# Performance work log

Measured on AMD Instinct MI355X. Metric: run time of the kernel, lower is better.

The kernel has to match this reference:

```python
import jax, jax.numpy as jnp
import numpy as np

NSAMPLE = 16
LEAKY_RATE = 0.1


def _knn(xyz, k):
    # xyz: [B,N,3] -> idx of k nearest neighbors (incl. self): [B,N,k]
    sq = jnp.sum(xyz * xyz, axis=-1)  # [B,N]
    dist = sq[:, :, None] + sq[:, None, :] - 2.0 * jnp.einsum('bnd,bmd->bnm', xyz, xyz)
    _, idx = jax.lax.top_k(-dist, k)
    return idx


def _gather(feat, idx):
    # feat [B,N,C], idx [B,N,K] -> [B,N,K,C]
    return jax.vmap(lambda f, i: f[i])(feat, idx)


def setup_inputs() -> dict:
    key = jax.random.key(0)
    ks = jax.random.split(key, 10)
    B, N, D = 8, 4096, 61
    in_ch, out_ch, wnet = 64, 64, 16
    inp = {
        'xyz': jax.random.normal(ks[0], (B, 3, N), dtype=jnp.float32),
        'points': jax.random.normal(ks[1], (B, D, N), dtype=jnp.float32),
        # WeightNet: 1x1 convs 3->8->8->16 (hidden_unit=[8,8]), no BN
        'w0': jax.random.normal(ks[2], (8, 3), dtype=jnp.float32) * 0.3,
        'b0': jnp.zeros((8,), dtype=jnp.float32),
        'w1': jax.random.normal(ks[3], (8, 8), dtype=jnp.float32) * 0.3,
        'b1': jnp.zeros((8,), dtype=jnp.float32),
        'w2': jax.random.normal(ks[4], (wnet, 8), dtype=jnp.float32) * 0.3,
        'b2': jnp.zeros((wnet,), dtype=jnp.float32),
        # final Linear: weightnet*in_channel -> out_channel (torch [out,in] layout)
        'lin_w': jax.random.normal(ks[5], (out_ch, wnet * in_ch), dtype=jnp.float32) * 0.03,
        'lin_b': jnp.zeros((out_ch,), dtype=jnp.float32),
    }
    return inp


def reference(xyz, points, w0, b0, w1, b1, w2, b2, lin_w, lin_b):
    B, _, N = xyz.shape
    xyz_t = jnp.transpose(xyz, (0, 2, 1))     # [B,N,3]
    pts_t = jnp.transpose(points, (0, 2, 1))  # [B,N,D]
    idx = _knn(xyz_t, NSAMPLE)                # [B,N,K]
    g_xyz = _gather(xyz_t, idx) - xyz_t[:, :, None, :]   # [B,N,K,3] relative coords
    g_pts = _gather(pts_t, idx)                           # [B,N,K,D]
    new_points = jnp.concatenate([g_xyz, g_pts], axis=-1)  # [B,N,K,C], C=D+3
    # WeightNet: per-neighbor 1x1-conv MLP with ReLU on relative coords
    h = jax.nn.relu(jnp.einsum('bnkc,oc->bnko', g_xyz, w0) + b0)
    h = jax.nn.relu(jnp.einsum('bnkc,oc->bnko', h, w1) + b1)
    w = jax.nn.relu(jnp.einsum('bnkc,oc->bnko', h, w2) + b2)  # [B,N,K,W]
    # aggregate: [B,N,C,K] @ [B,N,K,W] -> [B,N,C,W] -> flatten C*W (W fastest)
    agg = jnp.einsum('bnkc,bnkw->bncw', new_points, w).reshape(B, N, -1)
    out = agg @ lin_w.T + lin_b          # [B,N,out_ch]
    out = jnp.transpose(out, (0, 2, 1))  # [B,out_ch,N]
    return jnp.where(out > 0, out, LEAKY_RATE * out)  # LeakyReLU(0.1)
```

## Files before the change

kernel.cpp:

```cpp
#include <hip/hip_runtime.h>
#include <hip/hip_bf16.h>

#define NBATCH 8
#define NP     4096
#define ND     61
#define NK     16
#define BN     (NBATCH*NP)

#define OFF_XYZT  0
#define OFF_IDX   (OFF_XYZT + BN*16)
#define OFF_PTST  (OFF_IDX + BN*64)
#define OFF_BFRAG (OFF_PTST + BN*256)

typedef __attribute__((ext_vector_type(8))) short bf16x8;
typedef __attribute__((ext_vector_type(4))) float f32x4;

static __device__ __forceinline__ unsigned short f2bf(float x) {
    unsigned int u = __float_as_uint(x);
    return (unsigned short)((u + 0x7fffu + ((u >> 16) & 1u)) >> 16);
}

__global__ __launch_bounds__(256) void k_prep(const float* __restrict__ xyz,
                                              const float* __restrict__ pts,
                                              const float* __restrict__ lw,
                                              float4* __restrict__ xyzt,
                                              float* __restrict__ ptst,
                                              uint4* __restrict__ bfrag) {
#pragma clang fp contract(off)
    __shared__ float tile[64][65];
    int blk = blockIdx.x;
    int tid = threadIdx.x;
    if (blk < 128) {
        int t = blk * 256 + tid;
        int b = t >> 12, n = t & (NP - 1);
        const float* base = xyz + (size_t)b * 3 * NP + n;
        float x = base[0], y = base[NP], z = base[2 * NP];
        float sq = ((x * x) + (y * y)) + (z * z);
        xyzt[t] = make_float4(x, y, z, sq);
    } else if (blk < 640) {
        int bb = blk - 128;
        int b = bb >> 6; int n0 = (bb & 63) << 6;
        int rg = tid >> 6; int cl = tid & 63;
#pragma unroll
        for (int d0 = 0; d0 < 64; d0 += 4) {
            int d = d0 + rg;
            if (d < ND) tile[d][cl] = pts[((size_t)b * ND + d) * NP + n0 + cl];
        }
        __syncthreads();
#pragma unroll
        for (int r = 0; r < 16; ++r) {
            int n1 = r * 4 + rg;
            float v = (cl < ND) ? tile[cl][n1] : 0.0f;
            ptst[((size_t)b * NP + n0 + n1) * 64 + cl] = v;
        }
    } else {
        int e = (blk - 640) * 256 + tid;
        int lane = e & 63, nt = (e >> 6) & 3, ks = e >> 8;
        int k0 = ks * 32 + (lane >> 4) * 8;
        int n = nt * 16 + (lane & 15);
        const float* src = lw + (size_t)n * 1024 + k0;
        unsigned int pk[4];
#pragma unroll
        for (int i = 0; i < 4; ++i)
            pk[i] = ((unsigned int)f2bf(src[2 * i + 1]) << 16) | f2bf(src[2 * i]);
        bfrag[e] = make_uint4(pk[0], pk[1], pk[2], pk[3]);
    }
}

#define INSERT16(dv, jv)                                            \
    do {                                                            \
        bd[15] = (dv); bi[15] = (jv);                               \
        _Pragma("unroll")                                           \
        for (int s_ = 15; s_ > 0; --s_) {                           \
            bool sw_ = bd[s_] < bd[s_ - 1];                         \
            float td_ = bd[s_]; int ti_ = bi[s_];                   \
            bd[s_]     = sw_ ? bd[s_ - 1] : td_;                    \
            bi[s_]     = sw_ ? bi[s_ - 1] : ti_;                    \
            bd[s_ - 1] = sw_ ? td_ : bd[s_ - 1];                    \
            bi[s_ - 1] = sw_ ? ti_ : bi[s_ - 1];                    \
        }                                                           \
    } while (0)

#define DRAIN16(basev)                                                        \
    do {                                                                      \
        for (int r_ = 0; r_ < 16; ++r_) {                                     \
            if (!__any(r_ < cnt)) break;                                      \
            if (r_ < cnt) {                                                   \
                int loc_ = ring[r_ * 64 + lane];                              \
                float4 cd_ = tile[loc_];                                      \
                float dot_ = __fadd_rn(__fadd_rn(__fmul_rn(cd_.x, me.x),      \
                                                 __fmul_rn(cd_.y, me.y)),     \
                                       __fmul_rn(cd_.z, me.z));               \
                float dist_ = __fsub_rn(__fadd_rn(me.w, cd_.w),               \
                                        __fmul_rn(2.0f, dot_));               \
                if (dist_ < bd[15]) {                                         \
                    int gj_ = (basev) + loc_;                                 \
                    INSERT16(dist_, gj_);                                     \
                }                                                             \
            }                                                                 \
        }                                                                     \
        cnt = 0;                                                              \
        T = fminf(T, (bd[15] - me.w) + 1.0e-3f);                              \
    } while (0)

#define TSYNC()                                                               \
    do {                                                                      \
        Tsh[w * 64 + lane] = bd[15];                                          \
        float tm_ = Tsh[lane];                                                \
        _Pragma("unroll")                                                     \
        for (int v_ = 1; v_ < 8; ++v_) tm_ = fminf(tm_, Tsh[v_ * 64 + lane]); \
        T = fminf(T, (tm_ - me.w) + 1.0e-3f);                                 \
    } while (0)

__global__ __launch_bounds__(512) void k_knn(const float4* __restrict__ xyzt,
                                             int* __restrict__ out) {
    __shared__ char smem[51200];
    int tid = threadIdx.x;
    int w = tid >> 6, lane = tid & 63;
    int blk = blockIdx.x;
    int b = blk >> 6;
    int qbase = (blk & 63) << 6;
    const float4* xb = xyzt + (size_t)b * NP;

    float4* tile = (float4*)(smem + w * 4096);
    unsigned short* ring = (unsigned short*)(smem + 32768 + w * 2048);
    float* Tsh = (float*)(smem + 49152);

    float4 me = xb[qbase + lane];
    float bd[16]; int bi[16];
#pragma unroll
    for (int i = 0; i < 16; ++i) { bd[i] = 3.0e38f; bi[i] = 0; }
    int cnt = 0;
    float T = 3.0e38f;
    Tsh[w * 64 + lane] = 3.0e38f;
    __syncthreads();

    int cbase = w * 512;
    for (int half = 0; half < 2; ++half) {
        int base = cbase + half * 256;
#pragma unroll
        for (int r = 0; r < 4; ++r)
            tile[lane + r * 64] = xb[base + lane + r * 64];
        for (int seg = 0; seg < 4; ++seg) {
            for (int g = 0; g < 8; ++g) {
                int j0 = seg * 64 + g * 8;
#pragma unroll
                for (int u = 0; u < 8; ++u) {
                    int jj = j0 + u;
                    float4 cd = tile[jj];
                    float dotf = fmaf(cd.z, me.z, fmaf(cd.y, me.y, cd.x * me.x));
                    float df = fmaf(-2.0f, dotf, cd.w);
                    if (df < T) { ring[cnt * 64 + lane] = (unsigned short)jj; ++cnt; }
                }
                if (__any(cnt >= 8)) { DRAIN16(base); }
                if (half == 0 && seg == 0 && (g == 1 || g == 3)) { TSYNC(); }
            }
            TSYNC();
        }
        DRAIN16(base);
    }

    __syncthreads();
    float2* part = (float2*)smem;
    if (w < 4) {
#pragma unroll
        for (int e = 0; e < 16; ++e)
            part[(w * 16 + e) * 64 + lane] = make_float2(bd[e], __int_as_float(bi[e]));
    }
    __syncthreads();
    if (w == 0) {
        for (int s = 1; s < 4; ++s) {
#pragma unroll
            for (int e = 0; e < 16; ++e) {
                float2 v = part[(s * 16 + e) * 64 + lane];
                if (v.x >= bd[15]) break;
                float d_ = v.x; int j_ = __float_as_int(v.y);
                INSERT16(d_, j_);
            }
        }
    }
    __syncthreads();
    if (w >= 4) {
#pragma unroll
        for (int e = 0; e < 16; ++e)
            part[((w - 4) * 16 + e) * 64 + lane] = make_float2(bd[e], __int_as_float(bi[e]));
    }
    __syncthreads();
    if (w == 0) {
        for (int s = 0; s < 4; ++s) {
#pragma unroll
            for (int e = 0; e < 16; ++e) {
                float2 v = part[(s * 16 + e) * 64 + lane];
                if (v.x >= bd[15]) break;
                float d_ = v.x; int j_ = __float_as_int(v.y);
                INSERT16(d_, j_);
            }
        }
        int4* op = (int4*)(out + ((size_t)b * NP + qbase + lane) * 16);
        op[0] = make_int4(bi[0], bi[1], bi[2], bi[3]);
        op[1] = make_int4(bi[4], bi[5], bi[6], bi[7]);
        op[2] = make_int4(bi[8], bi[9], bi[10], bi[11]);
        op[3] = make_int4(bi[12], bi[13], bi[14], bi[15]);
    }
}

__global__ __launch_bounds__(256) void k_wagg(
    const float4* __restrict__ xyzt, const int* __restrict__ knn,
    const float* __restrict__ ptst, const uint4* __restrict__ bfrag,
    const float* __restrict__ w0, const float* __restrict__ b0,
    const float* __restrict__ w1, const float* __restrict__ b1,
    const float* __restrict__ w2, const float* __restrict__ b2,
    const float* __restrict__ linb, float* __restrict__ out) {
    __shared__ float wkl[256 * 16];
    __shared__ float4 rel4[256];
    __shared__ uint4 aggL4[16 * 128];
    char* aggL = (char*)aggL4;

    int tid = threadIdx.x;
    int wid = tid >> 6, lane = tid & 63;
    int q0 = blockIdx.x * 16;
    int b = q0 >> 12;
    int n0 = q0 & (NP - 1);
    size_t bN = (size_t)b * NP;

    {
        int pw = lane >> 4, k = lane & 15;
        int p = wid * 4 + pw;
        int r = p * 16 + k;
        int q = q0 + p;
        int j = knn[(size_t)q * 16 + k];
        float4 pj = xyzt[bN + j];
        float4 pq = xyzt[q];
        float rx = pj.x - pq.x, ry = pj.y - pq.y, rz = pj.z - pq.z;
        float h0[8], h1[8], wv[16];
#pragma unroll
        for (int o = 0; o < 8; ++o) {
            float a = w0[o * 3 + 0] * rx + w0[o * 3 + 1] * ry + w0[o * 3 + 2] * rz + b0[o];
            h0[o] = a > 0.0f ? a : 0.0f;
        }
#pragma unroll
        for (int o = 0; o < 8; ++o) {
            float a = b1[o];
#pragma unroll
            for (int c2 = 0; c2 < 8; ++c2) a += w1[o * 8 + c2] * h0[c2];
            h1[o] = a > 0.0f ? a : 0.0f;
        }
#pragma unroll
        for (int o = 0; o < 16; ++o) {
            float a = b2[o];
#pragma unroll
            for (int c2 = 0; c2 < 8; ++c2) a += w2[o * 8 + c2] * h1[c2];
            wv[o] = a > 0.0f ? a : 0.0f;
        }
        int f = (r >> 1) & 3;
#pragma unroll
        for (int s = 0; s < 4; ++s)
            *(float4*)&wkl[r * 16 + ((s ^ f) << 2)] =
                make_float4(wv[s * 4], wv[s * 4 + 1], wv[s * 4 + 2], wv[s * 4 + 3]);
        rel4[r] = make_float4(rx, ry, rz, __int_as_float(j));
    }
    __syncthreads();

    for (int u = 0; u < 4; ++u) {
        int p = wid * 4 + u;
        float acc[16];
#pragma unroll
        for (int w = 0; w < 16; ++w) acc[w] = 0.0f;
#pragma unroll
        for (int kh = 0; kh < 2; ++kh) {
            float vv[8];
#pragma unroll
            for (int kk = 0; kk < 8; ++kk) {
                int r = p * 16 + kh * 8 + kk;
                float4 rj = rel4[r];
                int j = __float_as_int(rj.w);
                vv[kk] = (lane >= 3) ? ptst[(bN + j) * 64 + (lane - 3)]
                                     : ((lane == 0) ? rj.x : ((lane == 1) ? rj.y : rj.z));
            }
#pragma unroll
            for (int kk = 0; kk < 8; ++kk) {
                int r = p * 16 + kh * 8 + kk;
                int f = (r >> 1) & 3;
                float v = vv[kk];
#pragma unroll
                for (int s = 0; s < 4; ++s) {
                    float4 wv4 = *(const float4*)&wkl[r * 16 + ((s ^ f) << 2)];
                    acc[s * 4 + 0] = fmaf(v, wv4.x, acc[s * 4 + 0]);
                    acc[s * 4 + 1] = fmaf(v, wv4.y, acc[s * 4 + 1]);
                    acc[s * 4 + 2] = fmaf(v, wv4.z, acc[s * 4 + 2]);
                    acc[s * 4 + 3] = fmaf(v, wv4.w, acc[s * 4 + 3]);
                }
            }
        }
        unsigned int pk[8];
#pragma unroll
        for (int i = 0; i < 8; ++i)
            pk[i] = ((unsigned int)f2bf(acc[2 * i + 1]) << 16) | f2bf(acc[2 * i]);
        int cx = lane ^ (p & 7);
        *(uint4*)&aggL[p * 2048 + cx * 16]        = make_uint4(pk[0], pk[1], pk[2], pk[3]);
        *(uint4*)&aggL[p * 2048 + 1024 + cx * 16] = make_uint4(pk[4], pk[5], pk[6], pk[7]);
    }
    __syncthreads();

    f32x4 cacc = {0.0f, 0.0f, 0.0f, 0.0f};
    {
        int p_ = lane & 15, oct = lane >> 4;
        int h = oct & 1, chalf = oct >> 1;
        int pbase = p_ * 2048 + h * 1024;
        int px = p_ & 7;
#pragma unroll 4
        for (int ks = 0; ks < 32; ++ks) {
            int c = ks * 2 + chalf;
            bf16x8 av = *(const bf16x8*)&aggL[pbase + ((c ^ px) << 4)];
            bf16x8 bv = *(const bf16x8*)&bfrag[(ks * 4 + wid) * 64 + lane];
            cacc = __builtin_amdgcn_mfma_f32_16x16x32_bf16(av, bv, cacc, 0, 0, 0);
        }
    }
    __syncthreads();
    float* cout = wkl;
    {
        int o = wid * 16 + (lane & 15);
        int rbase = (lane >> 4) * 4;
#pragma unroll
        for (int reg = 0; reg < 4; ++reg)
            cout[o * 17 + rbase + reg] = cacc[reg];
    }
    __syncthreads();
    {
        int oo = tid >> 2, pq = tid & 3;
        float bias = linb[oo];
        float res[4];
#pragma unroll
        for (int e = 0; e < 4; ++e) {
            float s = cout[oo * 17 + pq * 4 + e] + bias;
            res[e] = s > 0.0f ? s : 0.1f * s;
        }
        *(float4*)&out[((size_t)(b * 64 + oo)) * NP + n0 + pq * 4] =
            make_float4(res[0], res[1], res[2], res[3]);
    }
}

extern "C" void kernel_launch(void* const* d_in, const int* in_sizes, int n_in,
                              void* d_out, int out_size, void* d_ws, size_t ws_size,
                              hipStream_t stream) {
    const float* xyz  = (const float*)d_in[0];
    const float* pts  = (const float*)d_in[1];
    const float* w0   = (const float*)d_in[2];
    const float* b0   = (const float*)d_in[3];
    const float* w1   = (const float*)d_in[4];
    const float* b1   = (const float*)d_in[5];
    const float* w2   = (const float*)d_in[6];
    const float* b2   = (const float*)d_in[7];
    const float* lw   = (const float*)d_in[8];
    const float* linb = (const float*)d_in[9];
    float* out = (float*)d_out;

    char* ws = (char*)d_ws;
    float4* xyzt  = (float4*)(ws + OFF_XYZT);
    int*    idx   = (int*)(ws + OFF_IDX);
    float*  ptst  = (float*)(ws + OFF_PTST);
    uint4*  bfrag = (uint4*)(ws + OFF_BFRAG);

    k_prep<<<672, 256, 0, stream>>>(xyz, pts, lw, xyzt, ptst, bfrag);
    k_knn<<<512, 512, 0, stream>>>(xyzt, idx);
    k_wagg<<<BN / 16, 256, 0, stream>>>(xyzt, idx, ptst, bfrag,
                                        w0, b0, w1, b1, w2, b2, linb, out);
    (void)in_sizes; (void)n_in; (void)out_size; (void)ws_size;
}
```

Measured before the change: 222.8 us.

## Fuse kNN search with weightnet aggregation and linear into one kernel

Merges the kNN kernel and the weight/aggregate/MFMA kernel into a single 512-thread block that keeps the 64 queries' neighbor indices in shared memory as 16-bit values and processes them in four 16-query chunks. This removes the global index write/read and one kernel launch. In exchange, the aggregation phase runs on a grid of only 512 blocks, with half the waves idle during weightnet and MFMA. The candidate insertion in the scan loop is also changed to an unconditional ring write with a predicated counter increment, to avoid divergent branches.

```diff
diff --git a/kernel.cpp b/kernel.cpp
--- a/kernel.cpp
+++ b/kernel.cpp
@@ -112,231 +112,230 @@
         T = fminf(T, (tm_ - me.w) + 1.0e-3f);                                 \
     } while (0)
 
-__global__ __launch_bounds__(512) void k_knn(const float4* __restrict__ xyzt,
-                                             int* __restrict__ out) {
-    __shared__ char smem[51200];
-    int tid = threadIdx.x;
-    int w = tid >> 6, lane = tid & 63;
-    int blk = blockIdx.x;
-    int b = blk >> 6;
-    int qbase = (blk & 63) << 6;
-    const float4* xb = xyzt + (size_t)b * NP;
-
-    float4* tile = (float4*)(smem + w * 4096);
-    unsigned short* ring = (unsigned short*)(smem + 32768 + w * 2048);
-    float* Tsh = (float*)(smem + 49152);
-
-    float4 me = xb[qbase + lane];
-    float bd[16]; int bi[16];
-#pragma unroll
-    for (int i = 0; i < 16; ++i) { bd[i] = 3.0e38f; bi[i] = 0; }
-    int cnt = 0;
-    float T = 3.0e38f;
-    Tsh[w * 64 + lane] = 3.0e38f;
-    __syncthreads();
-
-    int cbase = w * 512;
-    for (int half = 0; half < 2; ++half) {
-        int base = cbase + half * 256;
-#pragma unroll
-        for (int r = 0; r < 4; ++r)
-            tile[lane + r * 64] = xb[base + lane + r * 64];
-        for (int seg = 0; seg < 4; ++seg) {
-            for (int g = 0; g < 8; ++g) {
-                int j0 = seg * 64 + g * 8;
-#pragma unroll
-                for (int u = 0; u < 8; ++u) {
-                    int jj = j0 + u;
-                    float4 cd = tile[jj];
-                    float dotf = fmaf(cd.z, me.z, fmaf(cd.y, me.y, cd.x * me.x));
-                    float df = fmaf(-2.0f, dotf, cd.w);
-                    if (df < T) { ring[cnt * 64 + lane] = (unsigned short)jj; ++cnt; }
-                }
-                if (__any(cnt >= 8)) { DRAIN16(base); }
-                if (half == 0 && seg == 0 && (g == 1 || g == 3)) { TSYNC(); }
-            }
-            TSYNC();
-        }
-        DRAIN16(base);
-    }
-
-    __syncthreads();
-    float2* part = (float2*)smem;
-    if (w < 4) {
-#pragma unroll
-        for (int e = 0; e < 16; ++e)
-            part[(w * 16 + e) * 64 + lane] = make_float2(bd[e], __int_as_float(bi[e]));
-    }
-    __syncthreads();
-    if (w == 0) {
-        for (int s = 1; s < 4; ++s) {
-#pragma unroll
-            for (int e = 0; e < 16; ++e) {
-                float2 v = part[(s * 16 + e) * 64 + lane];
-                if (v.x >= bd[15]) break;
-                float d_ = v.x; int j_ = __float_as_int(v.y);
-                INSERT16(d_, j_);
-            }
-        }
-    }
-    __syncthreads();
-    if (w >= 4) {
-#pragma unroll
-        for (int e = 0; e < 16; ++e)
-            part[((w - 4) * 16 + e) * 64 + lane] = make_float2(bd[e], __int_as_float(bi[e]));
-    }
-    __syncthreads();
-    if (w == 0) {
-        for (int s = 0; s < 4; ++s) {
-#pragma unroll
-            for (int e = 0; e < 16; ++e) {
-                float2 v = part[(s * 16 + e) * 64 + lane];
-                if (v.x >= bd[15]) break;
-                float d_ = v.x; int j_ = __float_as_int(v.y);
-                INSERT16(d_, j_);
-            }
-        }
-        int4* op = (int4*)(out + ((size_t)b * NP + qbase + lane) * 16);
-        op[0] = make_int4(bi[0], bi[1], bi[2], bi[3]);
-        op[1] = make_int4(bi[4], bi[5], bi[6], bi[7]);
-        op[2] = make_int4(bi[8], bi[9], bi[10], bi[11]);
-        op[3] = make_int4(bi[12], bi[13], bi[14], bi[15]);
-    }
-}
-
-__global__ __launch_bounds__(256) void k_wagg(
-    const float4* __restrict__ xyzt, const int* __restrict__ knn,
-    const float* __restrict__ ptst, const uint4* __restrict__ bfrag,
+__global__ __launch_bounds__(512, 4) void k_fused(
+    const float4* __restrict__ xyzt, const float* __restrict__ ptst,
+    const uint4* __restrict__ bfrag,
     const float* __restrict__ w0, const float* __restrict__ b0,
     const float* __restrict__ w1, const float* __restrict__ b1,
     const float* __restrict__ w2, const float* __restrict__ b2,
     const float* __restrict__ linb, float* __restrict__ out) {
-    __shared__ float wkl[256 * 16];
-    __shared__ float4 rel4[256];
-    __shared__ uint4 aggL4[16 * 128];
-    char* aggL = (char*)aggL4;
-
+    __shared__ char smem[54272];
     int tid = threadIdx.x;
-    int wid = tid >> 6, lane = tid & 63;
-    int q0 = blockIdx.x * 16;
-    int b = q0 >> 12;
-    int n0 = q0 & (NP - 1);
+    int blk = blockIdx.x;
+    int w = tid >> 6, lane = tid & 63;
+    int b = blk >> 6;
+    int qbase = (blk & 63) << 6;
+    const float4* xb = xyzt + (size_t)b * NP;
     size_t bN = (size_t)b * NP;
+    unsigned short* idxL = (unsigned short*)(smem + 52224);
 
     {
-        int pw = lane >> 4, k = lane & 15;
-        int p = wid * 4 + pw;
-        int r = p * 16 + k;
-        int q = q0 + p;
-        int j = knn[(size_t)q * 16 + k];
-        float4 pj = xyzt[bN + j];
-        float4 pq = xyzt[q];
-        float rx = pj.x - pq.x, ry = pj.y - pq.y, rz = pj.z - pq.z;
-        float h0[8], h1[8], wv[16];
-#pragma unroll
-        for (int o = 0; o < 8; ++o) {
-            float a = w0[o * 3 + 0] * rx + w0[o * 3 + 1] * ry + w0[o * 3 + 2] * rz + b0[o];
-            h0[o] = a > 0.0f ? a : 0.0f;
-        }
-#pragma unroll
-        for (int o = 0; o < 8; ++o) {
-            float a = b1[o];
-#pragma unroll
-            for (int c2 = 0; c2 < 8; ++c2) a += w1[o * 8 + c2] * h0[c2];
-            h1[o] = a > 0.0f ? a : 0.0f;
-        }
-#pragma unroll
-        for (int o = 0; o < 16; ++o) {
-            float a = b2[o];
-#pragma unroll
-            for (int c2 = 0; c2 < 8; ++c2) a += w2[o * 8 + c2] * h1[c2];
-            wv[o] = a > 0.0f ? a : 0.0f;
-        }
-        int f = (r >> 1) & 3;
-#pragma unroll
-        for (int s = 0; s < 4; ++s)
-            *(float4*)&wkl[r * 16 + ((s ^ f) << 2)] =
-                make_float4(wv[s * 4], wv[s * 4 + 1], wv[s * 4 + 2], wv[s * 4 + 3]);
-        rel4[r] = make_float4(rx, ry, rz, __int_as_float(j));
+        float4* tile = (float4*)(smem + w * 4096);
+        unsigned short* ring = (unsigned short*)(smem + 32768 + w * 2048);
+        float* Tsh = (float*)(smem + 49152);
+
+        float4 me = xb[qbase + lane];
+        float bd[16]; int bi[16];
+#pragma unroll
+        for (int i = 0; i < 16; ++i) { bd[i] = 3.0e38f; bi[i] = 0; }
+        int cnt = 0;
+        float T = 3.0e38f;
+        Tsh[w * 64 + lane] = 3.0e38f;
+        __syncthreads();
+
+        int cbase = w * 512;
+        for (int half = 0; half < 2; ++half) {
+            int base = cbase + half * 256;
+#pragma unroll
+            for (int r = 0; r < 4; ++r)
+                tile[lane + r * 64] = xb[base + lane + r * 64];
+            for (int seg = 0; seg < 4; ++seg) {
+                for (int g = 0; g < 8; ++g) {
+                    int j0 = seg * 64 + g * 8;
+#pragma unroll
+                    for (int u = 0; u < 8; ++u) {
+                        int jj = j0 + u;
+                        float4 cd = tile[jj];
+                        float dotf = fmaf(cd.z, me.z, fmaf(cd.y, me.y, cd.x * me.x));
+                        float df = fmaf(-2.0f, dotf, cd.w);
+                        ring[cnt * 64 + lane] = (unsigned short)jj;
+                        cnt += (df < T) ? 1 : 0;
+                    }
+                    if (__any(cnt >= 8)) { DRAIN16(base); }
+                    if (half == 0 && seg == 0 && (g == 1 || g == 3)) { TSYNC(); }
+                }
+                TSYNC();
+            }
+            DRAIN16(base);
+        }
+
+        __syncthreads();
+        float2* part = (float2*)smem;
+        if (w < 4) {
+#pragma unroll
+            for (int e = 0; e < 16; ++e)
+                part[(w * 16 + e) * 64 + lane] = make_float2(bd[e], __int_as_float(bi[e]));
+        }
+        __syncthreads();
+        if (w == 0) {
+            for (int s = 1; s < 4; ++s) {
+#pragma unroll
+                for (int e = 0; e < 16; ++e) {
+                    float2 v = part[(s * 16 + e) * 64 + lane];
+                    if (v.x >= bd[15]) break;
+                    float d_ = v.x; int j_ = __float_as_int(v.y);
+                    INSERT16(d_, j_);
+                }
+            }
+        }
+        __syncthreads();
+        if (w >= 4) {
+#pragma unroll
+            for (int e = 0; e < 16; ++e)
+                part[((w - 4) * 16 + e) * 64 + lane] = make_float2(bd[e], __int_as_float(bi[e]));
+        }
+        __syncthreads();
+        if (w == 0) {
+            for (int s = 0; s < 4; ++s) {
+#pragma unroll
+                for (int e = 0; e < 16; ++e) {
+                    float2 v = part[(s * 16 + e) * 64 + lane];
+                    if (v.x >= bd[15]) break;
+                    float d_ = v.x; int j_ = __float_as_int(v.y);
+                    INSERT16(d_, j_);
+                }
+            }
+#pragma unroll
+            for (int e = 0; e < 16; ++e)
+                idxL[lane * 16 + e] = (unsigned short)bi[e];
+        }
     }
     __syncthreads();
 
-    for (int u = 0; u < 4; ++u) {
-        int p = wid * 4 + u;
-        float acc[16];
-#pragma unroll
-        for (int w = 0; w < 16; ++w) acc[w] = 0.0f;
-#pragma unroll
-        for (int kh = 0; kh < 2; ++kh) {
-            float vv[8];
-#pragma unroll
-            for (int kk = 0; kk < 8; ++kk) {
-                int r = p * 16 + kh * 8 + kk;
-                float4 rj = rel4[r];
-                int j = __float_as_int(rj.w);
-                vv[kk] = (lane >= 3) ? ptst[(bN + j) * 64 + (lane - 3)]
-                                     : ((lane == 0) ? rj.x : ((lane == 1) ? rj.y : rj.z));
-            }
-#pragma unroll
-            for (int kk = 0; kk < 8; ++kk) {
-                int r = p * 16 + kh * 8 + kk;
-                int f = (r >> 1) & 3;
-                float v = vv[kk];
-#pragma unroll
-                for (int s = 0; s < 4; ++s) {
-                    float4 wv4 = *(const float4*)&wkl[r * 16 + ((s ^ f) << 2)];
-                    acc[s * 4 + 0] = fmaf(v, wv4.x, acc[s * 4 + 0]);
-                    acc[s * 4 + 1] = fmaf(v, wv4.y, acc[s * 4 + 1]);
-                    acc[s * 4 + 2] = fmaf(v, wv4.z, acc[s * 4 + 2]);
-                    acc[s * 4 + 3] = fmaf(v, wv4.w, acc[s * 4 + 3]);
-                }
-            }
-        }
-        unsigned int pk[8];
-#pragma unroll
-        for (int i = 0; i < 8; ++i)
-            pk[i] = ((unsigned int)f2bf(acc[2 * i + 1]) << 16) | f2bf(acc[2 * i]);
-        int cx = lane ^ (p & 7);
-        *(uint4*)&aggL[p * 2048 + cx * 16]        = make_uint4(pk[0], pk[1], pk[2], pk[3]);
-        *(uint4*)&aggL[p * 2048 + 1024 + cx * 16] = make_uint4(pk[4], pk[5], pk[6], pk[7]);
-    }
-    __syncthreads();
-
-    f32x4 cacc = {0.0f, 0.0f, 0.0f, 0.0f};
-    {
-        int p_ = lane & 15, oct = lane >> 4;
-        int h = oct & 1, chalf = oct >> 1;
-        int pbase = p_ * 2048 + h * 1024;
-        int px = p_ & 7;
+    float* wkl  = (float*)smem;
+    float* relx = (float*)(smem + 16384);
+    float* rely = (float*)(smem + 17408);
+    float* relz = (float*)(smem + 18432);
+    char*  aggL = smem + 19456;
+
+    for (int c = 0; c < 4; ++c) {
+        int n0 = qbase + c * 16;
+
+        if (tid < 256) {
+            int pw = lane >> 4, k = lane & 15;
+            int p = (tid >> 6) * 4 + pw;
+            int r = p * 16 + k;
+            int j = idxL[(c * 16 + p) * 16 + k];
+            float4 pj = xb[j];
+            float4 pq = xb[n0 + p];
+            float rx = pj.x - pq.x, ry = pj.y - pq.y, rz = pj.z - pq.z;
+            float h0[8], h1[8], wv[16];
+#pragma unroll
+            for (int o = 0; o < 8; ++o) {
+                float a = w0[o * 3 + 0] * rx + w0[o * 3 + 1] * ry + w0[o * 3 + 2] * rz + b0[o];
+                h0[o] = a > 0.0f ? a : 0.0f;
+            }
+#pragma unroll
+            for (int o = 0; o < 8; ++o) {
+                float a = b1[o];
+#pragma unroll
+                for (int c2 = 0; c2 < 8; ++c2) a += w1[o * 8 + c2] * h0[c2];
+                h1[o] = a > 0.0f ? a : 0.0f;
+            }
+#pragma unroll
+            for (int o = 0; o < 16; ++o) {
+                float a = b2[o];
+#pragma unroll
+                for (int c2 = 0; c2 < 8; ++c2) a += w2[o * 8 + c2] * h1[c2];
+                wv[o] = a > 0.0f ? a : 0.0f;
+            }
+            int f = (r >> 1) & 3;
+#pragma unroll
+            for (int s = 0; s < 4; ++s)
+                *(float4*)&wkl[r * 16 + ((s ^ f) << 2)] =
+                    make_float4(wv[s * 4], wv[s * 4 + 1], wv[s * 4 + 2], wv[s * 4 + 3]);
+            relx[r] = rx; rely[r] = ry; relz[r] = rz;
+        }
+        __syncthreads();
+
+        for (int u = 0; u < 2; ++u) {
+            int p = w * 2 + u;
+            float acc[16];
+#pragma unroll
+            for (int q = 0; q < 16; ++q) acc[q] = 0.0f;
+#pragma unroll
+            for (int kh = 0; kh < 2; ++kh) {
+                float vv[8];
+#pragma unroll
+                for (int kk = 0; kk < 8; ++kk) {
+                    int r = p * 16 + kh * 8 + kk;
+                    int j = idxL[(c * 16 + p) * 16 + kh * 8 + kk];
+                    vv[kk] = (lane >= 3) ? ptst[(bN + j) * 64 + (lane - 3)]
+                                         : ((lane == 0) ? relx[r]
+                                                        : ((lane == 1) ? rely[r] : relz[r]));
+                }
+#pragma unroll
+                for (int kk = 0; kk < 8; ++kk) {
+                    int r = p * 16 + kh * 8 + kk;
+                    int f = (r >> 1) & 3;
+                    float v = vv[kk];
+#pragma unroll
+                    for (int s = 0; s < 4; ++s) {
+                        float4 wv4 = *(const float4*)&wkl[r * 16 + ((s ^ f) << 2)];
+                        acc[s * 4 + 0] = fmaf(v, wv4.x, acc[s * 4 + 0]);
+                        acc[s * 4 + 1] = fmaf(v, wv4.y, acc[s * 4 + 1]);
+                        acc[s * 4 + 2] = fmaf(v, wv4.z, acc[s * 4 + 2]);
+                        acc[s * 4 + 3] = fmaf(v, wv4.w, acc[s * 4 + 3]);
+                    }
+                }
+            }
+            unsigned int pk[8];
+#pragma unroll
+            for (int i = 0; i < 8; ++i)
+                pk[i] = ((unsigned int)f2bf(acc[2 * i + 1]) << 16) | f2bf(acc[2 * i]);
+            int cx = lane ^ (p & 7);
+            *(uint4*)&aggL[p * 2048 + cx * 16]        = make_uint4(pk[0], pk[1], pk[2], pk[3]);
+            *(uint4*)&aggL[p * 2048 + 1024 + cx * 16] = make_uint4(pk[4], pk[5], pk[6], pk[7]);
+        }
+        __syncthreads();
+
+        f32x4 cacc = {0.0f, 0.0f, 0.0f, 0.0f};
+        if (w < 4) {
+            int p_ = lane & 15, oct = lane >> 4;
+            int h = oct & 1, chalf = oct >> 1;
+            int pbase = p_ * 2048 + h * 1024;
+            int px = p_ & 7;
 #pragma unroll 4
-        for (int ks = 0; ks < 32; ++ks) {
-            int c = ks * 2 + chalf;
-            bf16x8 av = *(const bf16x8*)&aggL[pbase + ((c ^ px) << 4)];
-            bf16x8 bv = *(const bf16x8*)&bfrag[(ks * 4 + wid) * 64 + lane];
-            cacc = __builtin_amdgcn_mfma_f32_16x16x32_bf16(av, bv, cacc, 0, 0, 0);
-        }
-    }
-    __syncthreads();
-    float* cout = wkl;
-    {
-        int o = wid * 16 + (lane & 15);
-        int rbase = (lane >> 4) * 4;
-#pragma unroll
-        for (int reg = 0; reg < 4; ++reg)
-            cout[o * 17 + rbase + reg] = cacc[reg];
-    }
-    __syncthreads();
-    {
-        int oo = tid >> 2, pq = tid & 3;
-        float bias = linb[oo];
-        float res[4];
-#pragma unroll
-        for (int e = 0; e < 4; ++e) {
-            float s = cout[oo * 17 + pq * 4 + e] + bias;
-            res[e] = s > 0.0f ? s : 0.1f * s;
-        }
-        *(float4*)&out[((size_t)(b * 64 + oo)) * NP + n0 + pq * 4] =
-            make_float4(res[0], res[1], res[2], res[3]);
+            for (int ks = 0; ks < 32; ++ks) {
+                int cc = ks * 2 + chalf;
+                bf16x8 av = *(const bf16x8*)&aggL[pbase + ((cc ^ px) << 4)];
+                bf16x8 bv = *(const bf16x8*)&bfrag[(ks * 4 + w) * 64 + lane];
+                cacc = __builtin_amdgcn_mfma_f32_16x16x32_bf16(av, bv, cacc, 0, 0, 0);
+            }
+        }
+        __syncthreads();
+        float* cout = wkl;
+        if (w < 4) {
+            int o = w * 16 + (lane & 15);
+            int rbase = (lane >> 4) * 4;
+#pragma unroll
+            for (int reg = 0; reg < 4; ++reg)
+                cout[o * 17 + rbase + reg] = cacc[reg];
+        }
+        __syncthreads();
+        if (tid < 256) {
+            int oo = tid >> 2, pq = tid & 3;
+            float bias = linb[oo];
+            float res[4];
+#pragma unroll
+            for (int e = 0; e < 4; ++e) {
+                float s = cout[oo * 17 + pq * 4 + e] + bias;
+                res[e] = s > 0.0f ? s : 0.1f * s;
+            }
+            *(float4*)&out[((size_t)(b * 64 + oo)) * NP + n0 + pq * 4] =
+                make_float4(res[0], res[1], res[2], res[3]);
+        }
+        __syncthreads();
     }
 }
 
@@ -357,13 +356,11 @@
 
     char* ws = (char*)d_ws;
     float4* xyzt  = (float4*)(ws + OFF_XYZT);
-    int*    idx   = (int*)(ws + OFF_IDX);
     float*  ptst  = (float*)(ws + OFF_PTST);
     uint4*  bfrag = (uint4*)(ws + OFF_BFRAG);
 
     k_prep<<<672, 256, 0, stream>>>(xyz, pts, lw, xyzt, ptst, bfrag);
-    k_knn<<<512, 512, 0, stream>>>(xyzt, idx);
-    k_wagg<<<BN / 16, 256, 0, stream>>>(xyzt, idx, ptst, bfrag,
-                                        w0, b0, w1, b1, w2, b2, linb, out);
+    k_fused<<<512, 512, 0, stream>>>(xyzt, ptst, bfrag,
+                                     w0, b0, w1, b1, w2, b2, linb, out);
     (void)in_sizes; (void)n_in; (void)out_size; (void)ws_size;
 }
```

Result: slower. 333.6 us (+49.7%).
